# Kernel optimization log

Measured on AMD Instinct MI355X. Metric: run time of the kernel, lower is better.

The kernel has to match this reference:

```python
import jax, jax.numpy as jnp
import numpy as np


def setup_inputs() -> dict:
    key = jax.random.key(0)
    k0, k1, k2, k3, k4 = jax.random.split(key, 5)
    B, S, D, E, H = 2, 4096, 1024, 8, 512
    x = jax.random.normal(k0, (B, S, D), jnp.float32)
    w_router = jax.random.normal(k1, (D, E), jnp.float32) * (D ** -0.5)
    w1 = jax.random.normal(k2, (E, D, H), jnp.float32) * (D ** -0.5)
    w2 = jax.random.normal(k3, (E, H, D), jnp.float32) * (H ** -0.5)
    w3 = jax.random.normal(k4, (E, D, H), jnp.float32) * (D ** -0.5)
    return {"x": x, "w_router": w_router, "w1": w1, "w2": w2, "w3": w3, "top_k": 2}


def reference(x, w_router, w1, w2, w3, top_k):
    """MoE layer: linear router -> softmax -> top_k, then grouped SwiGLU experts
    combined with the routing weights. out = sum_k w_k * Expert_{idx_k}(x)."""
    B, S, D = x.shape
    E = w_router.shape[1]
    xt = x.reshape(-1, D)                              # [T, D]
    T = xt.shape[0]

    # Router
    logits = xt @ w_router                             # [T, E]
    probs = jax.nn.softmax(logits, axis=-1)
    weights, idx = jax.lax.top_k(probs, top_k)         # [T, k], [T, k]

    # Scatter top-k weights into a dense per-token gate over experts.
    gate = jnp.zeros((T, E), xt.dtype).at[jnp.arange(T)[:, None], idx].add(weights)

    h = jax.nn.silu(jnp.einsum('td,edh->teh', xt, w1)) * jnp.einsum('td,edh->teh', xt, w3)
    y = jnp.einsum('te,teh,ehd->td', gate, h, w2)      # combine
    return y.reshape(B, S, D)
```

## Files before the change

kernel.cpp:

```cpp
#include <hip/hip_runtime.h>

#define NT    8192
#define DIM   1024
#define NE    8
#define NH    512
#define NROWS (NT*2)

typedef _Float16 f16;
typedef unsigned int u32;
typedef __attribute__((ext_vector_type(8))) _Float16 f16x8;
typedef __attribute__((ext_vector_type(4))) _Float16 f16x4;
typedef __attribute__((ext_vector_type(2))) _Float16 f16x2;
typedef __attribute__((ext_vector_type(4))) float f32x4;

__device__ __forceinline__ void gl2lds16(const f16* gptr, f16* ldsptr) {
    __builtin_amdgcn_global_load_lds(
        (const __attribute__((address_space(1))) u32*)gptr,
        (__attribute__((address_space(3))) u32*)ldsptr, 16, 0, 0);
}

#define FR(sbuf, row, q) \
    (*(const f16x8*)&sbuf[(row)*32 + (((q) ^ (((row) >> 1) & 3)) << 3)])

#define KC 512
__global__ __launch_bounds__(256) void prep_kernel(
    const float* __restrict__ x, const float* __restrict__ wr,
    const float* __restrict__ w1, const float* __restrict__ w3,
    const float* __restrict__ w2, float* __restrict__ plogits,
    f16* __restrict__ x16,
    f16* __restrict__ w1t, f16* __restrict__ w3t, f16* __restrict__ w2t,
    int* __restrict__ zint)
{
    __shared__ float smem[NE*KC];
    int tid = threadIdx.x;
    int bi = blockIdx.x;
    if (bi == 0 && tid < 16) zint[tid] = 0;
    if (bi < 1024) {
        int bx = bi & 511, by = bi >> 9;
        int kc0 = by * KC;
        for (int i = tid; i < NE*KC; i += 256) {
            int k = i >> 3, e = i & 7;
            smem[e*KC + k] = wr[(size_t)kc0*NE + i];
        }
        __syncthreads();
        int tok = bx*16 + (tid >> 4);
        int kl  = tid & 15;
        float acc[NE];
        #pragma unroll
        for (int e = 0; e < NE; e++) acc[e] = 0.f;
        const float* xrow = x + (size_t)tok*DIM + kc0;
        f16* xhrow = x16 + (size_t)tok*DIM + kc0;
        #pragma unroll
        for (int i = 0; i < KC/64; i++) {
            int kb = i*64 + kl*4;
            float4 xv = *(const float4*)(xrow + kb);
            f16x4 xh = { (f16)xv.x, (f16)xv.y, (f16)xv.z, (f16)xv.w };
            *(f16x4*)(xhrow + kb) = xh;
            #pragma unroll
            for (int e = 0; e < NE; e++) {
                float4 wv = *(const float4*)&smem[e*KC + kb];
                acc[e] += xv.x*wv.x + xv.y*wv.y + xv.z*wv.z + xv.w*wv.w;
            }
        }
        #pragma unroll
        for (int e = 0; e < NE; e++) {
            float v = acc[e];
            v += __shfl_xor(v, 1); v += __shfl_xor(v, 2);
            v += __shfl_xor(v, 4); v += __shfl_xor(v, 8);
            acc[e] = v;
        }
        if (kl == 0) {
            float* pp = plogits + ((size_t)by*NT + tok)*NE;
            float4 o0 = {acc[0], acc[1], acc[2], acc[3]};
            float4 o1 = {acc[4], acc[5], acc[6], acc[7]};
            *(float4*)pp = o0;
            *(float4*)(pp + 4) = o1;
        }
    } else {
        int tz = bi - 1024;
        int zx = tz & 127, zy = tz >> 7;
        int tensor = zy >> 3, e = zy & 7;
        const float* src; f16* dst; int R, C;
        if (tensor == 0)      { src = w1; dst = w1t; R = DIM; C = NH; }
        else if (tensor == 1) { src = w3; dst = w3t; R = DIM; C = NH; }
        else                  { src = w2; dst = w2t; R = NH; C = DIM; }
        src += (size_t)e * DIM * NH;
        dst += (size_t)e * DIM * NH;
        int tcols = C >> 6;
        int bx = zx % tcols, by = zx / tcols;
        int r0 = by*64, c0 = bx*64;
        #pragma unroll
        for (int p = 0; p < 4; p++) {
            int r = p*16 + (tid >> 4);
            int c = (tid & 15) << 2;
            float4 v = *(const float4*)&src[(size_t)(r0 + r)*C + c0 + c];
            *(float4*)&smem[r*64 + (c ^ (((r >> 3) & 7) << 2))] = v;
        }
        __syncthreads();
        #pragma unroll
        for (int pass = 0; pass < 2; pass++) {
            int s = pass*256 + tid;
            int h = s >> 3, a = s & 7, d0 = a << 3;
            int hs = h ^ (a << 2);
            f16x8 o;
            #pragma unroll
            for (int j = 0; j < 8; j++)
                o[j] = (f16)smem[(d0 + j)*64 + hs];
            *(f16x8*)&dst[(size_t)(c0 + h)*R + r0 + d0] = o;
        }
    }
}

__global__ __launch_bounds__(256) void route_kernel(
    const float* __restrict__ plogits, unsigned char* __restrict__ ge,
    float* __restrict__ gw, int* __restrict__ zint)
{
    __shared__ int lhist[NE];
    int tid = threadIdx.x;
    if (tid < NE) lhist[tid] = 0;
    __syncthreads();

    int t = blockIdx.x*256 + tid;
    const float* p0 = plogits + (size_t)t*NE;
    const float* p1 = plogits + (size_t)NT*NE + (size_t)t*NE;
    float4 a0 = *(const float4*)p0, a1 = *(const float4*)(p0+4);
    float4 b0 = *(const float4*)p1, b1 = *(const float4*)(p1+4);
    float l[NE] = { a0.x+b0.x, a0.y+b0.y, a0.z+b0.z, a0.w+b0.w,
                    a1.x+b1.x, a1.y+b1.y, a1.z+b1.z, a1.w+b1.w };
    float m = l[0];
    #pragma unroll
    for (int e = 1; e < NE; e++) m = fmaxf(m, l[e]);
    float s = 0.f;
    #pragma unroll
    for (int e = 0; e < NE; e++) { l[e] = __expf(l[e] - m); s += l[e]; }
    float inv = 1.f / s;
    int i0 = 0; float v0 = l[0];
    #pragma unroll
    for (int e = 1; e < NE; e++) if (l[e] > v0) { v0 = l[e]; i0 = e; }
    int i1 = -1; float v1 = -1.f;
    #pragma unroll
    for (int e = 0; e < NE; e++) if (e != i0 && l[e] > v1) { v1 = l[e]; i1 = e; }
    ge[2*t+0] = (unsigned char)i0; gw[2*t+0] = v0*inv;
    ge[2*t+1] = (unsigned char)i1; gw[2*t+1] = v1*inv;
    #pragma unroll
    for (int ee = 0; ee < NE; ee++) {
        int c = __popcll(__ballot(i0 == ee)) + __popcll(__ballot(i1 == ee));
        if ((tid & 63) == 0 && c) atomicAdd(&lhist[ee], c);
    }
    __syncthreads();
    if (tid < NE && lhist[tid]) atomicAdd(&zint[tid], lhist[tid]);
}

__global__ __launch_bounds__(256) void scatter_kernel(
    const unsigned char* __restrict__ ge, const float* __restrict__ gw,
    int* __restrict__ zint, int* __restrict__ offs, int* __restrict__ tok_ids,
    int* __restrict__ aid, float* __restrict__ row_gate)
{
    const int* ghist = zint;
    int* gcur = zint + 8;
    int tid = threadIdx.x;
    int loffs[NE]; int s = 0;
    #pragma unroll
    for (int e = 0; e < NE; e++) { loffs[e] = s; s += ghist[e]; }
    if (blockIdx.x == 0 && tid == 0) {
        #pragma unroll
        for (int e = 0; e < NE; e++) offs[e] = loffs[e];
        offs[NE] = s;
    }
    int id = blockIdx.x*256 + tid;
    int e = ge[id];
    float wv = gw[id];
    unsigned long long lt = (1ULL << (tid & 63)) - 1;
    int pos = 0;
    #pragma unroll
    for (int ee = 0; ee < NE; ee++) {
        unsigned long long mk = __ballot(e == ee);
        int cnt = __popcll(mk);
        int b = 0;
        if ((tid & 63) == 0 && cnt) b = atomicAdd(&gcur[ee], cnt);
        b = __shfl(b, 0);
        if (e == ee) pos = loffs[ee] + b + __popcll(mk & lt);
    }
    tok_ids[pos] = id >> 1;
    aid[pos] = id;
    row_gate[pos] = wv;
}


#define BM1 64
#define BN1 128
__global__ __launch_bounds__(256,3) void gemm1_kernel(
    const f16* __restrict__ x16, const int* __restrict__ tok_ids,
    const f16* __restrict__ w1t, const f16* __restrict__ w3t,
    f16* __restrict__ gbuf, const int* __restrict__ offs)
{
    int bi = blockIdx.x;
    int e  = bi & 7;
    int r_ = bi >> 3;
    int nt = r_ & 3;
    int mt = r_ >> 2;
    int off = offs[e];
    int n_e = offs[e+1] - off;
    if (mt*BM1 >= n_e) return;

    __shared__ f16 sA [2][BM1*32];
    __shared__ f16 sB1[2][BN1*32];
    __shared__ f16 sB3[2][BN1*32];
    __shared__ int stok[BM1];

    int tid = threadIdx.x;
    if (tid < BM1) {
        int rloc = mt*BM1 + tid; rloc = rloc < n_e ? rloc : n_e - 1;
        stok[tid] = tok_ids[off + rloc];
    }
    __syncthreads();

    int lane = tid & 63, w = tid >> 6;
    int wcol = w*32;
    int q = lane >> 4, lm = lane & 15;

    int arow = w*16 + (lane >> 2);
    int ag   = (lane & 3) ^ ((arow >> 1) & 3);
    const f16* pa = x16 + (size_t)stok[arow]*DIM + ag*8;
    const int la = w*512 + lane*8;

    int br0 = w*32 + (lane >> 2);
    int br1 = br0 + 16;
    int g0 = (lane & 3) ^ ((br0 >> 1) & 3);
    int g1 = (lane & 3) ^ ((br1 >> 1) & 3);
    const f16* w1p = w1t + ((size_t)e*NH + nt*BN1)*DIM;
    const f16* w3p = w3t + ((size_t)e*NH + nt*BN1)*DIM;
    const f16* pb1_0 = w1p + (size_t)br0*DIM + g0*8;
    const f16* pb1_1 = w1p + (size_t)br1*DIM + g1*8;
    const f16* pb3_0 = w3p + (size_t)br0*DIM + g0*8;
    const f16* pb3_1 = w3p + (size_t)br1*DIM + g1*8;
    const int lofs0 = br0*32 + ((lane & 3) << 3);
    const int lofs1 = br1*32 + ((lane & 3) << 3);

    f32x4 acc1[4][2], acc3[4][2];
    #pragma unroll
    for (int a = 0; a < 4; a++)
        #pragma unroll
        for (int b = 0; b < 2; b++) {
            acc1[a][b] = (f32x4){0.f,0.f,0.f,0.f};
            acc3[a][b] = (f32x4){0.f,0.f,0.f,0.f};
        }

    for (int k0 = 0; k0 < DIM; k0 += 64) {
        __syncthreads();
        gl2lds16(pa + k0,         &sA [0][la]);
        gl2lds16(pa + k0 + 32,    &sA [1][la]);
        gl2lds16(pb1_0 + k0,      &sB1[0][lofs0]);
        gl2lds16(pb1_1 + k0,      &sB1[0][lofs1]);
        gl2lds16(pb1_0 + k0 + 32, &sB1[1][lofs0]);
        gl2lds16(pb1_1 + k0 + 32, &sB1[1][lofs1]);
        gl2lds16(pb3_0 + k0,      &sB3[0][lofs0]);
        gl2lds16(pb3_1 + k0,      &sB3[0][lofs1]);
        gl2lds16(pb3_0 + k0 + 32, &sB3[1][lofs0]);
        gl2lds16(pb3_1 + k0 + 32, &sB3[1][lofs1]);
        __syncthreads();
        #pragma unroll
        for (int ks = 0; ks < 2; ks++) {
            f16x8 aF[4], b1F[2], b3F[2];
            #pragma unroll
            for (int s = 0; s < 4; s++) aF[s] = FR(sA[ks], s*16 + lm, q);
            #pragma unroll
            for (int c = 0; c < 2; c++) {
                b1F[c] = FR(sB1[ks], wcol + c*16 + lm, q);
                b3F[c] = FR(sB3[ks], wcol + c*16 + lm, q);
            }
            #pragma unroll
            for (int sr = 0; sr < 4; sr++)
                #pragma unroll
                for (int sc = 0; sc < 2; sc++) {
                    acc1[sr][sc] = __builtin_amdgcn_mfma_f32_16x16x32_f16(aF[sr], b1F[sc], acc1[sr][sc], 0, 0, 0);
                    acc3[sr][sc] = __builtin_amdgcn_mfma_f32_16x16x32_f16(aF[sr], b3F[sc], acc3[sr][sc], 0, 0, 0);
                }
        }
    }
    #pragma unroll
    for (int sr = 0; sr < 4; sr++) {
        #pragma unroll
        for (int reg = 0; reg < 4; reg++) {
            int row = mt*BM1 + sr*16 + q*4 + reg;
            if (row < n_e) {
                #pragma unroll
                for (int sc = 0; sc < 2; sc++) {
                    int col = nt*BN1 + wcol + sc*16 + lm;
                    float h1 = acc1[sr][sc][reg];
                    float h3 = acc3[sr][sc][reg];
                    float gv = h1 / (1.f + __expf(-h1)) * h3;
                    gbuf[(size_t)(off + row)*NH + col] = (f16)gv;
                }
            }
        }
    }
}

#define BM 128
#define BN 128
__global__ __launch_bounds__(256,3) void gemm2_kernel(
    const f16* __restrict__ gbuf, const f16* __restrict__ w2t,
    const int* __restrict__ offs, const int* __restrict__ aid,
    const float* __restrict__ row_gate, f16* __restrict__ ybuf)
{
    int bi = blockIdx.x;
    int e  = bi & 7;
    int r_ = bi >> 3;
    int nt = r_ & 7;
    int mt = r_ >> 3;
    int off = offs[e];
    int n_e = offs[e+1] - off;
    if (mt*BM >= n_e) return;

    __shared__ f16 sA[2][BM*32];
    __shared__ f16 sB[2][BN*32];
    __shared__ int said[BM];
    __shared__ float sgate[BM];

    int tid = threadIdx.x;
    if (tid < BM) {
        int rloc = mt*BM + tid;
        if (rloc < n_e) { said[tid] = aid[off + rloc]; sgate[tid] = row_gate[off + rloc]; }
        else            { said[tid] = 0; sgate[tid] = 0.f; }
    }

    int lane = tid & 63, w = tid >> 6;
    int wrow = (w >> 1)*64, wcol = (w & 1)*64;
    int q = lane >> 4, lm = lane & 15;

    int lr0 = w*32 + (lane >> 2);
    int lr1 = lr0 + 16;
    int g0 = (lane & 3) ^ ((lr0 >> 1) & 3);
    int g1 = (lane & 3) ^ ((lr1 >> 1) & 3);
    int ga0 = mt*BM + lr0; ga0 = ga0 < n_e ? ga0 : n_e - 1;
    int ga1 = mt*BM + lr1; ga1 = ga1 < n_e ? ga1 : n_e - 1;
    const f16* pA0 = gbuf + (size_t)(off + ga0)*NH + g0*8;
    const f16* pA1 = gbuf + (size_t)(off + ga1)*NH + g1*8;
    const f16* w2p = w2t + ((size_t)e*DIM + nt*BN)*NH;
    const f16* pB0 = w2p + (size_t)lr0*NH + g0*8;
    const f16* pB1 = w2p + (size_t)lr1*NH + g1*8;
    const int lofs0 = lr0*32 + ((lane & 3) << 3);
    const int lofs1 = lr1*32 + ((lane & 3) << 3);

    f32x4 acc[4][4];
    #pragma unroll
    for (int a = 0; a < 4; a++)
        #pragma unroll
        for (int b = 0; b < 4; b++) acc[a][b] = (f32x4){0.f,0.f,0.f,0.f};

    __syncthreads();

    for (int k0 = 0; k0 < NH; k0 += 64) {
        gl2lds16(pA0 + k0,      &sA[0][lofs0]);
        gl2lds16(pA1 + k0,      &sA[0][lofs1]);
        gl2lds16(pA0 + k0 + 32, &sA[1][lofs0]);
        gl2lds16(pA1 + k0 + 32, &sA[1][lofs1]);
        gl2lds16(pB0 + k0,      &sB[0][lofs0]);
        gl2lds16(pB1 + k0,      &sB[0][lofs1]);
        gl2lds16(pB0 + k0 + 32, &sB[1][lofs0]);
        gl2lds16(pB1 + k0 + 32, &sB[1][lofs1]);
        __syncthreads();
        #pragma unroll
        for (int ks = 0; ks < 2; ks++) {
            f16x8 aF[4], bF[4];
            #pragma unroll
            for (int s = 0; s < 4; s++) {
                aF[s] = FR(sA[ks], wrow + s*16 + lm, q);
                bF[s] = FR(sB[ks], wcol + s*16 + lm, q);
            }
            #pragma unroll
            for (int sr = 0; sr < 4; sr++)
                #pragma unroll
                for (int sc = 0; sc < 4; sc++)
                    acc[sr][sc] = __builtin_amdgcn_mfma_f32_16x16x32_f16(aF[sr], bF[sc], acc[sr][sc], 0, 0, 0);
        }
        __syncthreads();
    }
    #pragma unroll
    for (int sr = 0; sr < 4; sr++) {
        #pragma unroll
        for (int reg = 0; reg < 4; reg++) {
            int lrow = wrow + sr*16 + q*4 + reg;
            if (mt*BM + lrow < n_e) {
                int id = said[lrow];
                float wgt = sgate[lrow];
                #pragma unroll
                for (int sc = 0; sc < 4; sc++) {
                    int col = nt*BN + wcol + sc*16 + lm;
                    ybuf[(size_t)id*DIM + col] = (f16)(wgt * acc[sr][sc][reg]);
                }
            }
        }
    }
}

__global__ __launch_bounds__(256) void combine_kernel(
    const f16* __restrict__ ybuf, float* __restrict__ out)
{
    int gid = blockIdx.x*256 + threadIdx.x;
    int t = gid >> 7;
    int c = (gid & 127) << 3;
    f16x8 y0 = *(const f16x8*)(ybuf + ((size_t)2*t)*DIM + c);
    f16x8 y1 = *(const f16x8*)(ybuf + ((size_t)2*t+1)*DIM + c);
    float* op = out + (size_t)t*DIM + c;
    float4 o0 = { (float)y0[0] + (float)y1[0], (float)y0[1] + (float)y1[1],
                  (float)y0[2] + (float)y1[2], (float)y0[3] + (float)y1[3] };
    float4 o1 = { (float)y0[4] + (float)y1[4], (float)y0[5] + (float)y1[5],
                  (float)y0[6] + (float)y1[6], (float)y0[7] + (float)y1[7] };
    *(float4*)op = o0;
    *(float4*)(op + 4) = o1;
}

extern "C" void kernel_launch(void* const* d_in, const int* in_sizes, int n_in,
                              void* d_out, int out_size, void* d_ws, size_t ws_size,
                              hipStream_t stream)
{
    const float* x  = (const float*)d_in[0];
    const float* wr = (const float*)d_in[1];
    const float* w1 = (const float*)d_in[2];
    const float* w2 = (const float*)d_in[3];
    const float* w3 = (const float*)d_in[4];
    float* out = (float*)d_out;

    char* ws = (char*)d_ws;
    f16* ybuf    = (f16*)ws;        ws += (size_t)NROWS*DIM*sizeof(f16);
    f16* w1t     = (f16*)ws;        ws += (size_t)NE*NH*DIM*sizeof(f16);
    f16* w3t     = (f16*)ws;        ws += (size_t)NE*NH*DIM*sizeof(f16);
    f16* w2t     = (f16*)ws;        ws += (size_t)NE*DIM*NH*sizeof(f16);
    f16* gbuf    = (f16*)ws;        ws += (size_t)NROWS*NH*sizeof(f16);
    float* plogits = (float*)ws;    ws += (size_t)2*NT*NE*4;
    int* tok_ids = (int*)ws;        ws += (size_t)NROWS*4;
    int* aid     = (int*)ws;        ws += (size_t)NROWS*4;
    float* row_gate = (float*)ws;   ws += (size_t)NROWS*4;
    int* offs    = (int*)ws;        ws += 64;
    unsigned char* ge = (unsigned char*)ws; ws += (size_t)NROWS;
    float* gw    = (float*)ws;      ws += (size_t)NROWS*4;
    int* zint    = (int*)ws;        ws += 64;
    if (ws_size < (size_t)(ws - (char*)d_ws)) return;

    f16* x16 = ybuf;

    prep_kernel<<<1024 + 3072, 256, 0, stream>>>(x, wr, w1, w3, w2,
                                                 plogits, x16, w1t, w3t, w2t, zint);
    route_kernel<<<NT/256, 256, 0, stream>>>(plogits, ge, gw, zint);
    scatter_kernel<<<NROWS/256, 256, 0, stream>>>(ge, gw, zint, offs,
                                                  tok_ids, aid, row_gate);
    gemm1_kernel<<<8192, 256, 0, stream>>>(x16, tok_ids, w1t, w3t, gbuf, offs);
    gemm2_kernel<<<8192, 256, 0, stream>>>(gbuf, w2t, offs, aid, row_gate, ybuf);
    combine_kernel<<<(NT*(DIM/8))/256, 256, 0, stream>>>(ybuf, out);
}
```

Measured before the change: 241.0 us.

## Split gate GEMM into two 128x128 tiled kernels and atomically combine into output

After: 289.3 us. +20.1%, slower.

```diff
diff --git a/kernel.cpp b/kernel.cpp
--- a/kernel.cpp
+++ b/kernel.cpp
@@ -29,11 +29,17 @@
     const float* __restrict__ w2, float* __restrict__ plogits,
     f16* __restrict__ x16,
     f16* __restrict__ w1t, f16* __restrict__ w3t, f16* __restrict__ w2t,
-    int* __restrict__ zint)
+    int* __restrict__ zint, float* __restrict__ out)
 {
     __shared__ float smem[NE*KC];
     int tid = threadIdx.x;
     int bi = blockIdx.x;
+    {
+        float4 z = {0.f, 0.f, 0.f, 0.f};
+        float4* op = (float4*)out + (size_t)bi*512 + tid;
+        op[0] = z;
+        op[256] = z;
+    }
     if (bi == 0 && tid < 16) zint[tid] = 0;
     if (bi < 1024) {
         int bx = bi & 511, by = bi >> 9;
@@ -187,12 +193,12 @@
 }
 
 
-#define BM1 64
+#define BM1 128
 #define BN1 128
-__global__ __launch_bounds__(256,3) void gemm1_kernel(
+__global__ __launch_bounds__(256,3) void gemm1a_kernel(
     const f16* __restrict__ x16, const int* __restrict__ tok_ids,
-    const f16* __restrict__ w1t, const f16* __restrict__ w3t,
-    f16* __restrict__ gbuf, const int* __restrict__ offs)
+    const f16* __restrict__ w1t, f16* __restrict__ s1buf,
+    const int* __restrict__ offs)
 {
     int bi = blockIdx.x;
     int e  = bi & 7;
@@ -203,9 +209,8 @@
     int n_e = offs[e+1] - off;
     if (mt*BM1 >= n_e) return;
 
-    __shared__ f16 sA [2][BM1*32];
-    __shared__ f16 sB1[2][BN1*32];
-    __shared__ f16 sB3[2][BN1*32];
+    __shared__ f16 sA[2][BM1*32];
+    __shared__ f16 sB[2][BN1*32];
     __shared__ int stok[BM1];
 
     int tid = threadIdx.x;
@@ -216,80 +221,154 @@
     __syncthreads();
 
     int lane = tid & 63, w = tid >> 6;
-    int wcol = w*32;
+    int wrow = (w >> 1)*64, wcol = (w & 1)*64;
     int q = lane >> 4, lm = lane & 15;
 
-    int arow = w*16 + (lane >> 2);
-    int ag   = (lane & 3) ^ ((arow >> 1) & 3);
-    const f16* pa = x16 + (size_t)stok[arow]*DIM + ag*8;
-    const int la = w*512 + lane*8;
-
-    int br0 = w*32 + (lane >> 2);
-    int br1 = br0 + 16;
-    int g0 = (lane & 3) ^ ((br0 >> 1) & 3);
-    int g1 = (lane & 3) ^ ((br1 >> 1) & 3);
-    const f16* w1p = w1t + ((size_t)e*NH + nt*BN1)*DIM;
-    const f16* w3p = w3t + ((size_t)e*NH + nt*BN1)*DIM;
-    const f16* pb1_0 = w1p + (size_t)br0*DIM + g0*8;
-    const f16* pb1_1 = w1p + (size_t)br1*DIM + g1*8;
-    const f16* pb3_0 = w3p + (size_t)br0*DIM + g0*8;
-    const f16* pb3_1 = w3p + (size_t)br1*DIM + g1*8;
-    const int lofs0 = br0*32 + ((lane & 3) << 3);
-    const int lofs1 = br1*32 + ((lane & 3) << 3);
-
-    f32x4 acc1[4][2], acc3[4][2];
+    int lr0 = w*32 + (lane >> 2);
+    int lr1 = lr0 + 16;
+    int g0 = (lane & 3) ^ ((lr0 >> 1) & 3);
+    int g1 = (lane & 3) ^ ((lr1 >> 1) & 3);
+    const f16* pA0 = x16 + (size_t)stok[lr0]*DIM + g0*8;
+    const f16* pA1 = x16 + (size_t)stok[lr1]*DIM + g1*8;
+    const f16* wp  = w1t + ((size_t)e*NH + nt*BN1)*DIM;
+    const f16* pB0 = wp + (size_t)lr0*DIM + g0*8;
+    const f16* pB1 = wp + (size_t)lr1*DIM + g1*8;
+    const int l0 = lr0*32 + ((lane & 3) << 3);
+    const int l1 = lr1*32 + ((lane & 3) << 3);
+
+    f32x4 acc[4][4];
     #pragma unroll
     for (int a = 0; a < 4; a++)
         #pragma unroll
-        for (int b = 0; b < 2; b++) {
-            acc1[a][b] = (f32x4){0.f,0.f,0.f,0.f};
-            acc3[a][b] = (f32x4){0.f,0.f,0.f,0.f};
-        }
+        for (int b = 0; b < 4; b++) acc[a][b] = (f32x4){0.f,0.f,0.f,0.f};
 
     for (int k0 = 0; k0 < DIM; k0 += 64) {
-        __syncthreads();
-        gl2lds16(pa + k0,         &sA [0][la]);
-        gl2lds16(pa + k0 + 32,    &sA [1][la]);
-        gl2lds16(pb1_0 + k0,      &sB1[0][lofs0]);
-        gl2lds16(pb1_1 + k0,      &sB1[0][lofs1]);
-        gl2lds16(pb1_0 + k0 + 32, &sB1[1][lofs0]);
-        gl2lds16(pb1_1 + k0 + 32, &sB1[1][lofs1]);
-        gl2lds16(pb3_0 + k0,      &sB3[0][lofs0]);
-        gl2lds16(pb3_1 + k0,      &sB3[0][lofs1]);
-        gl2lds16(pb3_0 + k0 + 32, &sB3[1][lofs0]);
-        gl2lds16(pb3_1 + k0 + 32, &sB3[1][lofs1]);
+        gl2lds16(pA0 + k0,      &sA[0][l0]);
+        gl2lds16(pA1 + k0,      &sA[0][l1]);
+        gl2lds16(pA0 + k0 + 32, &sA[1][l0]);
+        gl2lds16(pA1 + k0 + 32, &sA[1][l1]);
+        gl2lds16(pB0 + k0,      &sB[0][l0]);
+        gl2lds16(pB1 + k0,      &sB[0][l1]);
+        gl2lds16(pB0 + k0 + 32, &sB[1][l0]);
+        gl2lds16(pB1 + k0 + 32, &sB[1][l1]);
         __syncthreads();
         #pragma unroll
         for (int ks = 0; ks < 2; ks++) {
-            f16x8 aF[4], b1F[2], b3F[2];
-            #pragma unroll
-            for (int s = 0; s < 4; s++) aF[s] = FR(sA[ks], s*16 + lm, q);
-            #pragma unroll
-            for (int c = 0; c < 2; c++) {
-                b1F[c] = FR(sB1[ks], wcol + c*16 + lm, q);
-                b3F[c] = FR(sB3[ks], wcol + c*16 + lm, q);
+            f16x8 aF[4], bF[4];
+            #pragma unroll
+            for (int s = 0; s < 4; s++) {
+                aF[s] = FR(sA[ks], wrow + s*16 + lm, q);
+                bF[s] = FR(sB[ks], wcol + s*16 + lm, q);
             }
             #pragma unroll
             for (int sr = 0; sr < 4; sr++)
                 #pragma unroll
-                for (int sc = 0; sc < 2; sc++) {
-                    acc1[sr][sc] = __builtin_amdgcn_mfma_f32_16x16x32_f16(aF[sr], b1F[sc], acc1[sr][sc], 0, 0, 0);
-                    acc3[sr][sc] = __builtin_amdgcn_mfma_f32_16x16x32_f16(aF[sr], b3F[sc], acc3[sr][sc], 0, 0, 0);
-                }
-        }
+                for (int sc = 0; sc < 4; sc++)
+                    acc[sr][sc] = __builtin_amdgcn_mfma_f32_16x16x32_f16(aF[sr], bF[sc], acc[sr][sc], 0, 0, 0);
+        }
+        __syncthreads();
     }
     #pragma unroll
     for (int sr = 0; sr < 4; sr++) {
         #pragma unroll
         for (int reg = 0; reg < 4; reg++) {
-            int row = mt*BM1 + sr*16 + q*4 + reg;
+            int row = mt*BM1 + wrow + sr*16 + q*4 + reg;
             if (row < n_e) {
                 #pragma unroll
-                for (int sc = 0; sc < 2; sc++) {
+                for (int sc = 0; sc < 4; sc++) {
                     int col = nt*BN1 + wcol + sc*16 + lm;
-                    float h1 = acc1[sr][sc][reg];
-                    float h3 = acc3[sr][sc][reg];
-                    float gv = h1 / (1.f + __expf(-h1)) * h3;
+                    float h1 = acc[sr][sc][reg];
+                    s1buf[(size_t)(off + row)*NH + col] = (f16)(h1 / (1.f + __expf(-h1)));
+                }
+            }
+        }
+    }
+}
+
+__global__ __launch_bounds__(256,3) void gemm1b_kernel(
+    const f16* __restrict__ x16, const int* __restrict__ tok_ids,
+    const f16* __restrict__ w3t, const f16* __restrict__ s1buf,
+    f16* __restrict__ gbuf, const int* __restrict__ offs)
+{
+    int bi = blockIdx.x;
+    int e  = bi & 7;
+    int r_ = bi >> 3;
+    int nt = r_ & 3;
+    int mt = r_ >> 2;
+    int off = offs[e];
+    int n_e = offs[e+1] - off;
+    if (mt*BM1 >= n_e) return;
+
+    __shared__ f16 sA[2][BM1*32];
+    __shared__ f16 sB[2][BN1*32];
+    __shared__ int stok[BM1];
+
+    int tid = threadIdx.x;
+    if (tid < BM1) {
+        int rloc = mt*BM1 + tid; rloc = rloc < n_e ? rloc : n_e - 1;
+        stok[tid] = tok_ids[off + rloc];
+    }
+    __syncthreads();
+
+    int lane = tid & 63, w = tid >> 6;
+    int wrow = (w >> 1)*64, wcol = (w & 1)*64;
+    int q = lane >> 4, lm = lane & 15;
+
+    int lr0 = w*32 + (lane >> 2);
+    int lr1 = lr0 + 16;
+    int g0 = (lane & 3) ^ ((lr0 >> 1) & 3);
+    int g1 = (lane & 3) ^ ((lr1 >> 1) & 3);
+    const f16* pA0 = x16 + (size_t)stok[lr0]*DIM + g0*8;
+    const f16* pA1 = x16 + (size_t)stok[lr1]*DIM + g1*8;
+    const f16* wp  = w3t + ((size_t)e*NH + nt*BN1)*DIM;
+    const f16* pB0 = wp + (size_t)lr0*DIM + g0*8;
+    const f16* pB1 = wp + (size_t)lr1*DIM + g1*8;
+    const int l0 = lr0*32 + ((lane & 3) << 3);
+    const int l1 = lr1*32 + ((lane & 3) << 3);
+
+    f32x4 acc[4][4];
+    #pragma unroll
+    for (int a = 0; a < 4; a++)
+        #pragma unroll
+        for (int b = 0; b < 4; b++) acc[a][b] = (f32x4){0.f,0.f,0.f,0.f};
+
+    for (int k0 = 0; k0 < DIM; k0 += 64) {
+        gl2lds16(pA0 + k0,      &sA[0][l0]);
+        gl2lds16(pA1 + k0,      &sA[0][l1]);
+        gl2lds16(pA0 + k0 + 32, &sA[1][l0]);
+        gl2lds16(pA1 + k0 + 32, &sA[1][l1]);
+        gl2lds16(pB0 + k0,      &sB[0][l0]);
+        gl2lds16(pB1 + k0,      &sB[0][l1]);
+        gl2lds16(pB0 + k0 + 32, &sB[1][l0]);
+        gl2lds16(pB1 + k0 + 32, &sB[1][l1]);
+        __syncthreads();
+        #pragma unroll
+        for (int ks = 0; ks < 2; ks++) {
+            f16x8 aF[4], bF[4];
+            #pragma unroll
+            for (int s = 0; s < 4; s++) {
+                aF[s] = FR(sA[ks], wrow + s*16 + lm, q);
+                bF[s] = FR(sB[ks], wcol + s*16 + lm, q);
+            }
+            #pragma unroll
+            for (int sr = 0; sr < 4; sr++)
+                #pragma unroll
+                for (int sc = 0; sc < 4; sc++)
+                    acc[sr][sc] = __builtin_amdgcn_mfma_f32_16x16x32_f16(aF[sr], bF[sc], acc[sr][sc], 0, 0, 0);
+        }
+        __syncthreads();
+    }
+    #pragma unroll
+    for (int sr = 0; sr < 4; sr++) {
+        #pragma unroll
+        for (int reg = 0; reg < 4; reg++) {
+            int row = mt*BM1 + wrow + sr*16 + q*4 + reg;
+            if (row < n_e) {
+                #pragma unroll
+                for (int sc = 0; sc < 4; sc++) {
+                    int col = nt*BN1 + wcol + sc*16 + lm;
+                    float s1 = (float)s1buf[(size_t)(off + row)*NH + col];
+                    float gv = s1 * acc[sr][sc][reg];
                     gbuf[(size_t)(off + row)*NH + col] = (f16)gv;
                 }
             }
@@ -302,7 +381,7 @@
 __global__ __launch_bounds__(256,3) void gemm2_kernel(
     const f16* __restrict__ gbuf, const f16* __restrict__ w2t,
     const int* __restrict__ offs, const int* __restrict__ aid,
-    const float* __restrict__ row_gate, f16* __restrict__ ybuf)
+    const float* __restrict__ row_gate, float* __restrict__ out)
 {
     int bi = blockIdx.x;
     int e  = bi & 7;
@@ -388,28 +467,12 @@
                 #pragma unroll
                 for (int sc = 0; sc < 4; sc++) {
                     int col = nt*BN + wcol + sc*16 + lm;
-                    ybuf[(size_t)id*DIM + col] = (f16)(wgt * acc[sr][sc][reg]);
+                    float v = (float)(f16)(wgt * acc[sr][sc][reg]);
+                    atomicAdd(&out[(size_t)(id >> 1)*DIM + col], v);
                 }
             }
         }
     }
-}
-
-__global__ __launch_bounds__(256) void combine_kernel(
-    const f16* __restrict__ ybuf, float* __restrict__ out)
-{
-    int gid = blockIdx.x*256 + threadIdx.x;
-    int t = gid >> 7;
-    int c = (gid & 127) << 3;
-    f16x8 y0 = *(const f16x8*)(ybuf + ((size_t)2*t)*DIM + c);
-    f16x8 y1 = *(const f16x8*)(ybuf + ((size_t)2*t+1)*DIM + c);
-    float* op = out + (size_t)t*DIM + c;
-    float4 o0 = { (float)y0[0] + (float)y1[0], (float)y0[1] + (float)y1[1],
-                  (float)y0[2] + (float)y1[2], (float)y0[3] + (float)y1[3] };
-    float4 o1 = { (float)y0[4] + (float)y1[4], (float)y0[5] + (float)y1[5],
-                  (float)y0[6] + (float)y1[6], (float)y0[7] + (float)y1[7] };
-    *(float4*)op = o0;
-    *(float4*)(op + 4) = o1;
 }
 
 extern "C" void kernel_launch(void* const* d_in, const int* in_sizes, int n_in,
@@ -424,7 +487,7 @@
     float* out = (float*)d_out;
 
     char* ws = (char*)d_ws;
-    f16* ybuf    = (f16*)ws;        ws += (size_t)NROWS*DIM*sizeof(f16);
+    f16* scratch = (f16*)ws;        ws += (size_t)NROWS*DIM*sizeof(f16);
     f16* w1t     = (f16*)ws;        ws += (size_t)NE*NH*DIM*sizeof(f16);
     f16* w3t     = (f16*)ws;        ws += (size_t)NE*NH*DIM*sizeof(f16);
     f16* w2t     = (f16*)ws;        ws += (size_t)NE*DIM*NH*sizeof(f16);
@@ -439,14 +502,16 @@
     int* zint    = (int*)ws;        ws += 64;
     if (ws_size < (size_t)(ws - (char*)d_ws)) return;
 
-    f16* x16 = ybuf;
+    f16* x16   = scratch;
+    f16* s1buf = scratch + (size_t)NT*DIM;
 
     prep_kernel<<<1024 + 3072, 256, 0, stream>>>(x, wr, w1, w3, w2,
-                                                 plogits, x16, w1t, w3t, w2t, zint);
+                                                 plogits, x16, w1t, w3t, w2t,
+                                                 zint, out);
     route_kernel<<<NT/256, 256, 0, stream>>>(plogits, ge, gw, zint);
     scatter_kernel<<<NROWS/256, 256, 0, stream>>>(ge, gw, zint, offs,
                                                   tok_ids, aid, row_gate);
-    gemm1_kernel<<<8192, 256, 0, stream>>>(x16, tok_ids, w1t, w3t, gbuf, offs);
-    gemm2_kernel<<<8192, 256, 0, stream>>>(gbuf, w2t, offs, aid, row_gate, ybuf);
-    combine_kernel<<<(NT*(DIM/8))/256, 256, 0, stream>>>(ybuf, out);
-}
+    gemm1a_kernel<<<4096, 256, 0, stream>>>(x16, tok_ids, w1t, s1buf, offs);
+    gemm1b_kernel<<<4096, 256, 0, stream>>>(x16, tok_ids, w3t, s1buf, gbuf, offs);
+    gemm2_kernel<<<8192, 256, 0, stream>>>(gbuf, w2t, offs, aid, row_gate, out);
+}
```
